# Kernel tuning notes

Measured on AMD Instinct MI355X. Metric: run time of the kernel, lower is better.

Reference implementation:

```python
import jax, jax.numpy as jnp
import numpy as np

N_ITER = 3  # routing iterations (init kwarg n_iter)


def _squash_elemwise(s):
    # Original squash sums squares over dim=-1, but s_j has a trailing
    # singleton dim there, so it degenerates to an elementwise map:
    # s^2/(1+s^2) * s/|s| == s*|s|/(1+s^2).
    return s * jnp.abs(s) / (1.0 + s * s)


def setup_inputs() -> dict:
    key = jax.random.key(0)
    k1, k2 = jax.random.split(key)
    B, R, C, O, I = 256, 1152, 10, 16, 8
    x = jax.random.normal(k1, (B, R, I), dtype=jnp.float32)
    W = jax.random.normal(k2, (R, C, O, I), dtype=jnp.float32)  # nn.Parameter (leading 1 dropped)
    return {"x": x, "W": W}


def reference(x, W):
    # u_hat[b,r,c,o] = sum_i W[r,c,o,i] * x[b,r,i]
    u_hat = jnp.einsum('rcoi,bri->brco', W, x)  # [B,R,C,O]
    R, C = u_hat.shape[1], u_hat.shape[2]
    b = jnp.zeros((R, C), dtype=u_hat.dtype)  # routing logits, shared across batch
    v = None
    for it in range(N_ITER):
        c = jax.nn.softmax(b, axis=0)                     # softmax over routes (dim=1 orig)
        s = jnp.einsum('rc,brco->bco', c, u_hat)          # weighted sum over routes
        v = _squash_elemwise(s)                           # [B,C,O]
        if it < N_ITER - 1:
            # agreement, mean over batch (b_ij is [1,R,C,1] in original)
            b = b + jnp.einsum('brco,bco->brc', u_hat, v).mean(axis=0)
    return v[..., None]  # matches v_j.squeeze(1): [B, n_capsules, out_ch, 1]
```

## Files before the change

kernel.cpp:

```cpp
#include <hip/hip_runtime.h>
#include <math.h>

namespace {
constexpr int NB = 256;
constexpr int NR = 1152;
constexpr int NC = 10;
constexpr int NO = 16;
constexpr int NI = 8;
constexpr int K1 = NR * NI;
constexpr int NN = NC * NO;
constexpr int KS = 8;
constexpr int KC = K1 / KS;
constexpr int RPB = NR / KS;
}

using s16x8 = __attribute__((ext_vector_type(8))) short;
using f32x4 = __attribute__((ext_vector_type(4))) float;

__device__ __forceinline__ ushort f2bf(float f) {
    uint u = __float_as_uint(f);
    uint r = (u + 0x7FFFu + ((u >> 16) & 1u)) >> 16;
    return (ushort)r;
}

__device__ __forceinline__ s16x8 pack8(float4 a0, float4 a1) {
    s16x8 r;
    r[0] = (short)f2bf(a0.x); r[1] = (short)f2bf(a0.y);
    r[2] = (short)f2bf(a0.z); r[3] = (short)f2bf(a0.w);
    r[4] = (short)f2bf(a1.x); r[5] = (short)f2bf(a1.y);
    r[6] = (short)f2bf(a1.z); r[7] = (short)f2bf(a1.w);
    return r;
}

__device__ __forceinline__ s16x8 pack8s(float4 a0, float4 a1, float cr) {
    s16x8 r;
    r[0] = (short)f2bf(a0.x * cr); r[1] = (short)f2bf(a0.y * cr);
    r[2] = (short)f2bf(a0.z * cr); r[3] = (short)f2bf(a0.w * cr);
    r[4] = (short)f2bf(a1.x * cr); r[5] = (short)f2bf(a1.y * cr);
    r[6] = (short)f2bf(a1.z * cr); r[7] = (short)f2bf(a1.w * cr);
    return r;
}

__device__ __forceinline__ s16x8 scale8(uint4 u, float cr) {
    s16x8 r;
    r[0] = (short)f2bf(__uint_as_float((u.x & 0xFFFFu) << 16) * cr);
    r[1] = (short)f2bf(__uint_as_float(u.x & 0xFFFF0000u) * cr);
    r[2] = (short)f2bf(__uint_as_float((u.y & 0xFFFFu) << 16) * cr);
    r[3] = (short)f2bf(__uint_as_float(u.y & 0xFFFF0000u) * cr);
    r[4] = (short)f2bf(__uint_as_float((u.z & 0xFFFFu) << 16) * cr);
    r[5] = (short)f2bf(__uint_as_float(u.z & 0xFFFF0000u) * cr);
    r[6] = (short)f2bf(__uint_as_float((u.w & 0xFFFFu) << 16) * cr);
    r[7] = (short)f2bf(__uint_as_float(u.w & 0xFFFF0000u) * cr);
    return r;
}

template <bool FIRST>
__global__ __launch_bounds__(256) void k_a(const float* __restrict__ x,
                                           const float* __restrict__ W,
                                           ushort* __restrict__ Wb,
                                           ushort* __restrict__ xbf,
                                           const float* __restrict__ bbuf,
                                           float* __restrict__ spart,
                                           ushort* __restrict__ xTbf) {
    const int m0 = blockIdx.x * 16;
    const int c  = blockIdx.y;
    const int ks = blockIdx.z;
    const int tid = threadIdx.x;
    const int w = tid >> 6, l = tid & 63;

    __shared__ float red[4][16][16];
    __shared__ float crs[RPB];
    __shared__ float sred[4], sred2[4];

    if constexpr (FIRST) {
        __shared__ __align__(16) ushort T[32][264];
        const int bid = blockIdx.x + 16 * blockIdx.y + 160 * blockIdx.z;
        if (bid < K1 / 32) {
            const int k0 = bid * 32;
            #pragma unroll
            for (int j = 0; j < 8; ++j) {
                int f  = j * 256 + tid;
                int b  = f >> 3;
                int i4 = f & 7;
                float4 v = *reinterpret_cast<const float4*>(
                    x + (size_t)b * K1 + k0 + i4 * 4);
                T[i4 * 4 + 0][b] = f2bf(v.x);
                T[i4 * 4 + 1][b] = f2bf(v.y);
                T[i4 * 4 + 2][b] = f2bf(v.z);
                T[i4 * 4 + 3][b] = f2bf(v.w);
            }
            __syncthreads();
            #pragma unroll
            for (int j = 0; j < 4; ++j) {
                int g   = j * 256 + tid;
                int row = g >> 5;
                int q8  = g & 31;
                *reinterpret_cast<uint4*>(xTbf + (size_t)(k0 + row) * NB + q8 * 8) =
                    *reinterpret_cast<const uint4*>(&T[row][q8 * 8]);
            }
        }
        const int nblk = 16 * NC * KS;
        const size_t gs = (size_t)(blockIdx.x + 16 * blockIdx.y + 160 * blockIdx.z) * 256 + tid;
        for (size_t e = gs; e < (size_t)NR * NC * NO; e += (size_t)nblk * 256) {
            float4 v0 = *reinterpret_cast<const float4*>(W + e * 8);
            float4 v1 = *reinterpret_cast<const float4*>(W + e * 8 + 4);
            s16x8 p = pack8(v0, v1);
            *reinterpret_cast<uint4*>(Wb + e * 8) = *reinterpret_cast<uint4*>(&p);
        }
        for (size_t e = gs; e < (size_t)NB * (K1 / 8); e += (size_t)nblk * 256) {
            float4 v0 = *reinterpret_cast<const float4*>(x + e * 8);
            float4 v1 = *reinterpret_cast<const float4*>(x + e * 8 + 4);
            s16x8 p = pack8(v0, v1);
            *reinterpret_cast<uint4*>(xbf + e * 8) = *reinterpret_cast<uint4*>(&p);
        }
    } else {
        float m = -1e30f;
        for (int r = tid; r < NR; r += 256) m = fmaxf(m, bbuf[r * NC + c]);
        #pragma unroll
        for (int off = 1; off < 64; off <<= 1) m = fmaxf(m, __shfl_xor(m, off));
        if (l == 0) sred[w] = m;
        __syncthreads();
        m = fmaxf(fmaxf(sred[0], sred[1]), fmaxf(sred[2], sred[3]));
        float s = 0.0f;
        for (int r = tid; r < NR; r += 256) s += expf(bbuf[r * NC + c] - m);
        #pragma unroll
        for (int off = 1; off < 64; off <<= 1) s += __shfl_xor(s, off);
        if (l == 0) sred2[w] = s;
        __syncthreads();
        s = sred2[0] + sred2[1] + sred2[2] + sred2[3];
        const float inv = 1.0f / s;
        for (int i = tid; i < RPB; i += 256)
            crs[i] = expf(bbuf[(ks * RPB + i) * NC + c] - m) * inv;
        __syncthreads();
    }

    const int kb = ks * KC + w * (KC / 4);
    const int lg = l >> 4;

    f32x4 acc = {0.f, 0.f, 0.f, 0.f};
    if constexpr (FIRST) {
        const float* ap = x + (size_t)(m0 + (l & 15)) * K1 + kb + 8 * lg;
        #pragma unroll
        for (int kk = 0; kk < KC / 4 / 32; ++kk) {
            const int k = kb + kk * 32 + 8 * lg;
            const int r = k >> 3;
            float4 a0 = *reinterpret_cast<const float4*>(ap + kk * 32);
            float4 a1 = *reinterpret_cast<const float4*>(ap + kk * 32 + 4);
            s16x8 a = pack8s(a0, a1, 1.0f / NR);
            const float* wp = W + ((size_t)r * NC + c) * 128 + (l & 15) * 8;
            s16x8 b = pack8(*reinterpret_cast<const float4*>(wp),
                            *reinterpret_cast<const float4*>(wp + 4));
            acc = __builtin_amdgcn_mfma_f32_16x16x32_bf16(a, b, acc, 0, 0, 0);
        }
    } else {
        const ushort* ap = xbf + (size_t)(m0 + (l & 15)) * K1 + kb + 8 * lg;
        #pragma unroll
        for (int kk = 0; kk < KC / 4 / 32; ++kk) {
            const int k = kb + kk * 32 + 8 * lg;
            const int r = k >> 3;
            uint4 ar = *reinterpret_cast<const uint4*>(ap + kk * 32);
            s16x8 a = scale8(ar, crs[r - ks * RPB]);
            s16x8 b = *reinterpret_cast<const s16x8*>(
                Wb + ((size_t)r * NC + c) * 128 + (l & 15) * 8);
            acc = __builtin_amdgcn_mfma_f32_16x16x32_bf16(a, b, acc, 0, 0, 0);
        }
    }

    #pragma unroll
    for (int q = 0; q < 4; ++q) red[w][4 * lg + q][l & 15] = acc[q];
    __syncthreads();
    const int row = tid >> 4, col = tid & 15;
    float s2 = red[0][row][col] + red[1][row][col]
             + red[2][row][col] + red[3][row][col];
    spart[(size_t)ks * (NB * NN) + (size_t)(m0 + row) * NN + c * NO + col] = s2;
}

__global__ __launch_bounds__(256) void k_b(const ushort* __restrict__ xTbf,
                                           const float* __restrict__ spart,
                                           const float* __restrict__ W,
                                           float* __restrict__ bbuf,
                                           int it) {
    const int c = blockIdx.y;
    const int tid = threadIdx.x;
    const int w = tid >> 6, l = tid & 63;

    __shared__ __align__(16) ushort VT[16][264];

    for (int f = tid; f < NB * NO; f += 256) {
        int b  = f >> 4;
        int oo = f & 15;
        size_t idx = (size_t)b * NN + c * NO + oo;
        float s = 0.0f;
        #pragma unroll
        for (int ks = 0; ks < KS; ++ks) s += spart[(size_t)ks * NB * NN + idx];
        float v = s * fabsf(s) / (1.0f + s * s);
        VT[oo][b] = f2bf(v);
    }
    __syncthreads();

    #pragma unroll
    for (int t = 0; t < 4; ++t) {
        const int mt = blockIdx.x * 16 + w * 4 + t;
        const int m0 = mt * 16;
        const ushort* ap = xTbf + (size_t)(m0 + (l & 15)) * NB + 8 * (l >> 4);
        f32x4 acc = {0.f, 0.f, 0.f, 0.f};
        #pragma unroll
        for (int kk = 0; kk < NB / 32; ++kk) {
            s16x8 a = *reinterpret_cast<const s16x8*>(ap + kk * 32);
            s16x8 b = *reinterpret_cast<const s16x8*>(&VT[l & 15][32 * kk + 8 * (l >> 4)]);
            acc = __builtin_amdgcn_mfma_f32_16x16x32_bf16(a, b, acc, 0, 0, 0);
        }
        const int h  = l >> 4, o = l & 15;
        const int r  = (m0 >> 3) + (h >> 1);
        const int i0 = (4 * h) & 7;
        const float4 w4 = *reinterpret_cast<const float4*>(
            W + (((size_t)r * NC + c) * NO + o) * NI + i0);
        float s = acc[0] * w4.x + acc[1] * w4.y + acc[2] * w4.z + acc[3] * w4.w;
        s += __shfl_xor(s, 1);
        s += __shfl_xor(s, 2);
        s += __shfl_xor(s, 4);
        s += __shfl_xor(s, 8);
        s += __shfl_xor(s, 16);
        if (l == 0 || l == 32) {
            int rr = (m0 >> 3) + (l >> 5);
            float val = s * (1.0f / NB);
            if (it > 0) bbuf[(size_t)rr * NC + c] += val;
            else        bbuf[(size_t)rr * NC + c] = val;
        }
    }
}

__global__ __launch_bounds__(256) void k_bf(const float* __restrict__ spart,
                                            float* __restrict__ out) {
    const int m0 = blockIdx.x * 16;
    const int c  = blockIdx.y;
    const int row = threadIdx.x >> 4, col = threadIdx.x & 15;
    size_t idx = (size_t)(m0 + row) * NN + c * NO + col;
    float s = 0.0f;
    #pragma unroll
    for (int ks = 0; ks < KS; ++ks) s += spart[(size_t)ks * NB * NN + idx];
    out[idx] = s * fabsf(s) / (1.0f + s * s);
}

extern "C" void kernel_launch(void* const* d_in, const int* in_sizes, int n_in,
                              void* d_out, int out_size, void* d_ws, size_t ws_size,
                              hipStream_t stream) {
    const float* x = (const float*)d_in[0];
    const float* W = (const float*)d_in[1];
    float* out = (float*)d_out;

    float*  spart = (float*)d_ws;
    float*  bbuf  = spart + (size_t)KS * NB * NN;
    ushort* xTbf  = (ushort*)(bbuf + (size_t)NR * NC);
    ushort* Wb    = xTbf + (size_t)K1 * NB;
    ushort* xbf   = Wb + (size_t)NR * NC * NO * NI;

    dim3 ga(NB / 16, NC, KS);
    dim3 gb(36, NC);
    dim3 gf(NB / 16, NC);

    k_a<true><<<ga, 256, 0, stream>>>(x, W, Wb, xbf, nullptr, spart, xTbf);
    k_b<<<gb, 256, 0, stream>>>(xTbf, spart, W, bbuf, 0);
    k_a<false><<<ga, 256, 0, stream>>>(x, W, Wb, xbf, bbuf, spart, nullptr);
    k_b<<<gb, 256, 0, stream>>>(xTbf, spart, W, bbuf, 1);
    k_a<false><<<ga, 256, 0, stream>>>(x, W, Wb, xbf, bbuf, spart, nullptr);
    k_bf<<<gf, 256, 0, stream>>>(spart, out);
}
```

Baseline: 80.60 us.

## Process two capsules per block in k_a and store routing logits transposed

Each k_a block now computes two capsule columns, so every loaded x tile (the A operand) is reused for two MFMA chains, and the grid is halved in y. The routing logits buffer is stored capsule-major so the per-capsule softmax reads are contiguous rather than strided by NC. The cost is more registers and shared memory per block, fewer blocks (640 instead of 1280), and a softmax prologue that runs twice in sequence.

```diff
diff --git a/kernel.cpp b/kernel.cpp
--- a/kernel.cpp
+++ b/kernel.cpp
@@ -59,22 +59,22 @@
                                            const float* __restrict__ W,
                                            ushort* __restrict__ Wb,
                                            ushort* __restrict__ xbf,
-                                           const float* __restrict__ bbuf,
+                                           const float* __restrict__ bbufT,
                                            float* __restrict__ spart,
                                            ushort* __restrict__ xTbf) {
     const int m0 = blockIdx.x * 16;
-    const int c  = blockIdx.y;
+    const int c0 = blockIdx.y * 2;
     const int ks = blockIdx.z;
     const int tid = threadIdx.x;
     const int w = tid >> 6, l = tid & 63;
 
-    __shared__ float red[4][16][16];
-    __shared__ float crs[RPB];
+    __shared__ float red[2][4][16][16];
+    __shared__ float crs[2][RPB];
     __shared__ float sred[4], sred2[4];
 
     if constexpr (FIRST) {
         __shared__ __align__(16) ushort T[32][264];
-        const int bid = blockIdx.x + 16 * blockIdx.y + 160 * blockIdx.z;
+        const int bid = blockIdx.x + 16 * blockIdx.y + 80 * blockIdx.z;
         if (bid < K1 / 32) {
             const int k0 = bid * 32;
             #pragma unroll
@@ -99,8 +99,8 @@
                     *reinterpret_cast<const uint4*>(&T[row][q8 * 8]);
             }
         }
-        const int nblk = 16 * NC * KS;
-        const size_t gs = (size_t)(blockIdx.x + 16 * blockIdx.y + 160 * blockIdx.z) * 256 + tid;
+        const int nblk = 16 * 5 * KS;
+        const size_t gs = (size_t)(blockIdx.x + 16 * blockIdx.y + 80 * blockIdx.z) * 256 + tid;
         for (size_t e = gs; e < (size_t)NR * NC * NO; e += (size_t)nblk * 256) {
             float4 v0 = *reinterpret_cast<const float4*>(W + e * 8);
             float4 v1 = *reinterpret_cast<const float4*>(W + e * 8 + 4);
@@ -114,71 +114,88 @@
             *reinterpret_cast<uint4*>(xbf + e * 8) = *reinterpret_cast<uint4*>(&p);
         }
     } else {
-        float m = -1e30f;
-        for (int r = tid; r < NR; r += 256) m = fmaxf(m, bbuf[r * NC + c]);
-        #pragma unroll
-        for (int off = 1; off < 64; off <<= 1) m = fmaxf(m, __shfl_xor(m, off));
-        if (l == 0) sred[w] = m;
-        __syncthreads();
-        m = fmaxf(fmaxf(sred[0], sred[1]), fmaxf(sred[2], sred[3]));
-        float s = 0.0f;
-        for (int r = tid; r < NR; r += 256) s += expf(bbuf[r * NC + c] - m);
-        #pragma unroll
-        for (int off = 1; off < 64; off <<= 1) s += __shfl_xor(s, off);
-        if (l == 0) sred2[w] = s;
-        __syncthreads();
-        s = sred2[0] + sred2[1] + sred2[2] + sred2[3];
-        const float inv = 1.0f / s;
-        for (int i = tid; i < RPB; i += 256)
-            crs[i] = expf(bbuf[(ks * RPB + i) * NC + c] - m) * inv;
-        __syncthreads();
+        #pragma unroll
+        for (int cc = 0; cc < 2; ++cc) {
+            const float* bc = bbufT + (size_t)(c0 + cc) * NR;
+            float m = -1e30f;
+            for (int r = tid; r < NR; r += 256) m = fmaxf(m, bc[r]);
+            #pragma unroll
+            for (int off = 1; off < 64; off <<= 1) m = fmaxf(m, __shfl_xor(m, off));
+            if (l == 0) sred[w] = m;
+            __syncthreads();
+            m = fmaxf(fmaxf(sred[0], sred[1]), fmaxf(sred[2], sred[3]));
+            float s = 0.0f;
+            for (int r = tid; r < NR; r += 256) s += expf(bc[r] - m);
+            #pragma unroll
+            for (int off = 1; off < 64; off <<= 1) s += __shfl_xor(s, off);
+            if (l == 0) sred2[w] = s;
+            __syncthreads();
+            s = sred2[0] + sred2[1] + sred2[2] + sred2[3];
+            const float inv = 1.0f / s;
+            for (int i = tid; i < RPB; i += 256)
+                crs[cc][i] = expf(bc[ks * RPB + i] - m) * inv;
+            __syncthreads();
+        }
     }
 
     const int kb = ks * KC + w * (KC / 4);
     const int lg = l >> 4;
 
-    f32x4 acc = {0.f, 0.f, 0.f, 0.f};
+    f32x4 acc0 = {0.f, 0.f, 0.f, 0.f};
+    f32x4 acc1 = {0.f, 0.f, 0.f, 0.f};
     if constexpr (FIRST) {
         const float* ap = x + (size_t)(m0 + (l & 15)) * K1 + kb + 8 * lg;
         #pragma unroll
         for (int kk = 0; kk < KC / 4 / 32; ++kk) {
-            const int k = kb + kk * 32 + 8 * lg;
-            const int r = k >> 3;
+            const int r = (kb + kk * 32 + 8 * lg) >> 3;
             float4 a0 = *reinterpret_cast<const float4*>(ap + kk * 32);
             float4 a1 = *reinterpret_cast<const float4*>(ap + kk * 32 + 4);
             s16x8 a = pack8s(a0, a1, 1.0f / NR);
-            const float* wp = W + ((size_t)r * NC + c) * 128 + (l & 15) * 8;
-            s16x8 b = pack8(*reinterpret_cast<const float4*>(wp),
-                            *reinterpret_cast<const float4*>(wp + 4));
-            acc = __builtin_amdgcn_mfma_f32_16x16x32_bf16(a, b, acc, 0, 0, 0);
+            const float* wp = W + ((size_t)r * NC + c0) * 128 + (l & 15) * 8;
+            s16x8 b0 = pack8(*reinterpret_cast<const float4*>(wp),
+                             *reinterpret_cast<const float4*>(wp + 4));
+            s16x8 b1 = pack8(*reinterpret_cast<const float4*>(wp + 128),
+                             *reinterpret_cast<const float4*>(wp + 132));
+            acc0 = __builtin_amdgcn_mfma_f32_16x16x32_bf16(a, b0, acc0, 0, 0, 0);
+            acc1 = __builtin_amdgcn_mfma_f32_16x16x32_bf16(a, b1, acc1, 0, 0, 0);
         }
     } else {
         const ushort* ap = xbf + (size_t)(m0 + (l & 15)) * K1 + kb + 8 * lg;
         #pragma unroll
         for (int kk = 0; kk < KC / 4 / 32; ++kk) {
-            const int k = kb + kk * 32 + 8 * lg;
-            const int r = k >> 3;
+            const int r  = (kb + kk * 32 + 8 * lg) >> 3;
+            const int ri = r - ks * RPB;
             uint4 ar = *reinterpret_cast<const uint4*>(ap + kk * 32);
-            s16x8 a = scale8(ar, crs[r - ks * RPB]);
-            s16x8 b = *reinterpret_cast<const s16x8*>(
-                Wb + ((size_t)r * NC + c) * 128 + (l & 15) * 8);
-            acc = __builtin_amdgcn_mfma_f32_16x16x32_bf16(a, b, acc, 0, 0, 0);
-        }
-    }
-
-    #pragma unroll
-    for (int q = 0; q < 4; ++q) red[w][4 * lg + q][l & 15] = acc[q];
+            s16x8 a0 = scale8(ar, crs[0][ri]);
+            s16x8 a1 = scale8(ar, crs[1][ri]);
+            const ushort* wp = Wb + ((size_t)r * NC + c0) * 128 + (l & 15) * 8;
+            s16x8 b0 = *reinterpret_cast<const s16x8*>(wp);
+            s16x8 b1 = *reinterpret_cast<const s16x8*>(wp + 128);
+            acc0 = __builtin_amdgcn_mfma_f32_16x16x32_bf16(a0, b0, acc0, 0, 0, 0);
+            acc1 = __builtin_amdgcn_mfma_f32_16x16x32_bf16(a1, b1, acc1, 0, 0, 0);
+        }
+    }
+
+    __syncthreads();
+    #pragma unroll
+    for (int q = 0; q < 4; ++q) {
+        red[0][w][4 * lg + q][l & 15] = acc0[q];
+        red[1][w][4 * lg + q][l & 15] = acc1[q];
+    }
     __syncthreads();
     const int row = tid >> 4, col = tid & 15;
-    float s2 = red[0][row][col] + red[1][row][col]
-             + red[2][row][col] + red[3][row][col];
-    spart[(size_t)ks * (NB * NN) + (size_t)(m0 + row) * NN + c * NO + col] = s2;
+    #pragma unroll
+    for (int cc = 0; cc < 2; ++cc) {
+        float s2 = red[cc][0][row][col] + red[cc][1][row][col]
+                 + red[cc][2][row][col] + red[cc][3][row][col];
+        spart[(size_t)ks * (NB * NN) + (size_t)(m0 + row) * NN + (c0 + cc) * NO + col] = s2;
+    }
 }
 
 __global__ __launch_bounds__(256) void k_b(const ushort* __restrict__ xTbf,
                                            const float* __restrict__ spart,
                                            const float* __restrict__ W,
-                                           float* __restrict__ bbuf,
+                                           float* __restrict__ bbufT,
                                            int it) {
     const int c = blockIdx.y;
     const int tid = threadIdx.x;
@@ -224,8 +241,8 @@
         if (l == 0 || l == 32) {
             int rr = (m0 >> 3) + (l >> 5);
             float val = s * (1.0f / NB);
-            if (it > 0) bbuf[(size_t)rr * NC + c] += val;
-            else        bbuf[(size_t)rr * NC + c] = val;
+            if (it > 0) bbufT[(size_t)c * NR + rr] += val;
+            else        bbufT[(size_t)c * NR + rr] = val;
         }
     }
 }
@@ -250,19 +267,19 @@
     float* out = (float*)d_out;
 
     float*  spart = (float*)d_ws;
-    float*  bbuf  = spart + (size_t)KS * NB * NN;
-    ushort* xTbf  = (ushort*)(bbuf + (size_t)NR * NC);
+    float*  bbufT = spart + (size_t)KS * NB * NN;
+    ushort* xTbf  = (ushort*)(bbufT + (size_t)NR * NC);
     ushort* Wb    = xTbf + (size_t)K1 * NB;
     ushort* xbf   = Wb + (size_t)NR * NC * NO * NI;
 
-    dim3 ga(NB / 16, NC, KS);
+    dim3 ga(NB / 16, NC / 2, KS);
     dim3 gb(36, NC);
     dim3 gf(NB / 16, NC);
 
     k_a<true><<<ga, 256, 0, stream>>>(x, W, Wb, xbf, nullptr, spart, xTbf);
-    k_b<<<gb, 256, 0, stream>>>(xTbf, spart, W, bbuf, 0);
-    k_a<false><<<ga, 256, 0, stream>>>(x, W, Wb, xbf, bbuf, spart, nullptr);
-    k_b<<<gb, 256, 0, stream>>>(xTbf, spart, W, bbuf, 1);
-    k_a<false><<<ga, 256, 0, stream>>>(x, W, Wb, xbf, bbuf, spart, nullptr);
+    k_b<<<gb, 256, 0, stream>>>(xTbf, spart, W, bbufT, 0);
+    k_a<false><<<ga, 256, 0, stream>>>(x, W, Wb, xbf, bbufT, spart, nullptr);
+    k_b<<<gb, 256, 0, stream>>>(xTbf, spart, W, bbufT, 1);
+    k_a<false><<<ga, 256, 0, stream>>>(x, W, Wb, xbf, bbufT, spart, nullptr);
     k_bf<<<gf, 256, 0, stream>>>(spart, out);
 }
```

Measured after the change: 78.71 us. 1.02x faster.
